# Kernel tuning notes

Measured on AMD Instinct MI355X. Metric: run time of the kernel, lower is better.

Reference implementation:

```python
import jax, jax.numpy as jnp
import numpy as np

SHAPES = ((8, 24, 24), (4, 12, 12), (2, 6, 6), (1, 3, 3))  # (D, H, W) per level
D_MODEL = 256
N_HEADS = 8
HEAD_DIM = D_MODEL // N_HEADS
N_LEVELS = 4
N_POINTS = 4
N_LAYERS = 6
D_FFN = 1024


def setup_inputs():
    key = jax.random.key(0)
    ks = iter(jax.random.split(key, 64))
    def rn(shape, s=1.0):
        return jax.random.normal(next(ks), shape, jnp.float32) * s
    inp = {}
    for i, (D, H, W) in enumerate(SHAPES):
        inp[f'src{i}'] = rn((2, 4, D_MODEL, D, H, W))
        inp[f'pos{i}'] = rn((2, 4, D_MODEL, D, H, W), 0.1)
    HLP3 = N_HEADS * N_LEVELS * N_POINTS * 3
    HLP = N_HEADS * N_LEVELS * N_POINTS
    L = N_LAYERS
    inp['level_embed'] = rn((N_LEVELS, D_MODEL), 0.02)
    inp['W_off'] = rn((L, D_MODEL, HLP3), 0.01)
    inp['b_off'] = rn((L, HLP3), 0.5)
    inp['W_attn'] = rn((L, D_MODEL, HLP), 0.02)
    inp['b_attn'] = jnp.zeros((L, HLP), jnp.float32)
    inp['W_val'] = rn((L, D_MODEL, D_MODEL), 0.02)
    inp['b_val'] = jnp.zeros((L, D_MODEL), jnp.float32)
    inp['W_out'] = rn((L, D_MODEL, D_MODEL), 0.02)
    inp['b_out'] = jnp.zeros((L, D_MODEL), jnp.float32)
    inp['g1'] = jnp.ones((L, D_MODEL), jnp.float32)
    inp['be1'] = jnp.zeros((L, D_MODEL), jnp.float32)
    inp['W1'] = rn((L, D_MODEL, D_FFN), 0.02)
    inp['b1'] = jnp.zeros((L, D_FFN), jnp.float32)
    inp['W2'] = rn((L, D_FFN, D_MODEL), 0.02)
    inp['b2'] = jnp.zeros((L, D_MODEL), jnp.float32)
    inp['g2'] = jnp.ones((L, D_MODEL), jnp.float32)
    inp['be2'] = jnp.zeros((L, D_MODEL), jnp.float32)
    return inp


def _layer_norm(x, g, b):
    m = jnp.mean(x, -1, keepdims=True)
    v = jnp.mean((x - m) ** 2, -1, keepdims=True)
    return (x - m) * jax.lax.rsqrt(v + 1e-5) * g + b


def _sample_level(v, loc, aw, D, H, W):
    # v: (B, nH, D*H*W, hd)   loc: (B, Lq, nH, P, 3) in [0,1] as (x,y,z)
    # aw: (B, Lq, nH, P) attention weights for this level
    # Trilinear sampling matching grid_sample(align_corners=False, padding_mode='zeros').
    B, Lq, nH, P, _ = loc.shape
    hd = v.shape[-1]
    x = loc[..., 0] * W - 0.5
    y = loc[..., 1] * H - 0.5
    z = loc[..., 2] * D - 0.5
    x0, y0, z0 = jnp.floor(x), jnp.floor(y), jnp.floor(z)
    fx, fy, fz = x - x0, y - y0, z - z0
    awt = aw.transpose(0, 2, 1, 3)  # (B, nH, Lq, P)
    out = jnp.zeros((B, nH, Lq, hd), v.dtype)
    for dz in (0, 1):
        for dy in (0, 1):
            for dx in (0, 1):
                xi, yi, zi = x0 + dx, y0 + dy, z0 + dz
                w = (fx if dx else 1.0 - fx) * (fy if dy else 1.0 - fy) * (fz if dz else 1.0 - fz)
                valid = (xi >= 0) & (xi < W) & (yi >= 0) & (yi < H) & (zi >= 0) & (zi < D)
                w = (w * valid).transpose(0, 2, 1, 3) * awt  # fold attn weight in
                idx = ((jnp.clip(zi, 0, D - 1) * H + jnp.clip(yi, 0, H - 1)) * W
                       + jnp.clip(xi, 0, W - 1)).astype(jnp.int32)
                idx = idx.transpose(0, 2, 1, 3).reshape(B, nH, Lq * P)
                g = jnp.take_along_axis(v, idx[..., None], 2).reshape(B, nH, Lq, P, hd)
                out = out + jnp.einsum('bhqpc,bhqp->bhqc', g, w)
    return out


def _msda(q, x, ref, Woff, boff, Wat, bat, Wv, bv, Wo, bo):
    B, Lq, _ = q.shape
    value = (x @ Wv + bv).reshape(B, Lq, N_HEADS, HEAD_DIM)
    off = (q @ Woff + boff).reshape(B, Lq, N_HEADS, N_LEVELS, N_POINTS, 3)
    attn = jax.nn.softmax((q @ Wat + bat).reshape(B, Lq, N_HEADS, N_LEVELS * N_POINTS), -1)
    attn = attn.reshape(B, Lq, N_HEADS, N_LEVELS, N_POINTS)
    # offset normalizer in (x, y, z) = (W, H, D) order per level
    norm = jnp.array([[W, H, D] for (D, H, W) in SHAPES], dtype=q.dtype)
    loc = ref[:, :, None, :, None, :] + off / norm[None, None, None, :, None, :]
    out = jnp.zeros((B, N_HEADS, Lq, HEAD_DIM), q.dtype)
    start = 0
    for lv, (D, H, W) in enumerate(SHAPES):
        n = D * H * W
        v_l = value[:, start:start + n].transpose(0, 2, 1, 3)  # (B, nH, n, hd)
        fn = jax.checkpoint(lambda v_, l_, a_, D=D, H=H, W=W: _sample_level(v_, l_, a_, D, H, W))
        out = out + fn(v_l, loc[:, :, :, lv], attn[:, :, :, lv])
        start += n
    return out.transpose(0, 2, 1, 3).reshape(B, Lq, D_MODEL) @ Wo + bo


def _forward(src0, src1, src2, src3, pos0, pos1, pos2, pos3, level_embed,
             W_off, b_off, W_attn, b_attn, W_val, b_val, W_out, b_out,
             g1, be1, W1, b1, W2, b2, g2, be2):
    srcs = [src0, src1, src2, src3]
    poss = [pos0, pos1, pos2, pos3]
    bs, nf = src0.shape[0], src0.shape[1]
    xs, ps = [], []
    for lvl in range(N_LEVELS):
        s, p = srcs[lvl], poss[lvl]
        b, n, c = s.shape[:3]
        xs.append(s.reshape(b, n, c, -1).transpose(0, 1, 3, 2))
        ps.append(p.reshape(b, n, c, -1).transpose(0, 1, 3, 2) + level_embed[lvl])
    x = jnp.concatenate(xs, 2)    # (bs, nf, Len, C)
    pos = jnp.concatenate(ps, 2)
    Len = x.shape[2]
    B = bs * nf
    x = x.reshape(B, Len, D_MODEL)
    pos = pos.reshape(B, Len, D_MODEL)
    # reference points; masks are all-False so valid_ratios == 1
    refs = []
    for (D, H, W) in SHAPES:
        rz, ry, rx = jnp.meshgrid(
            (jnp.arange(D, dtype=jnp.float32) + 0.5) / D,
            (jnp.arange(H, dtype=jnp.float32) + 0.5) / H,
            (jnp.arange(W, dtype=jnp.float32) + 0.5) / W,
            indexing='ij')
        refs.append(jnp.stack([rx.ravel(), ry.ravel(), rz.ravel()], -1))
    ref = jnp.concatenate(refs, 0)  # (Len, 3)
    ref = jnp.broadcast_to(ref[None, :, None, :], (B, Len, N_LEVELS, 3))
    for l in range(N_LAYERS):
        q = x + pos
        a = _msda(q, x, ref, W_off[l], b_off[l], W_attn[l], b_attn[l],
                  W_val[l], b_val[l], W_out[l], b_out[l])
        x = _layer_norm(x + a, g1[l], be1[l])
        ff = jax.nn.relu(x @ W1[l] + b1[l]) @ W2[l] + b2[l]
        x = _layer_norm(x + ff, g2[l], be2[l])
    return x.reshape(bs, nf, Len, D_MODEL)


def reference(src0, src1, src2, src3, pos0, pos1, pos2, pos3, level_embed,
              W_off, b_off, W_attn, b_attn, W_val, b_val, W_out, b_out,
              g1, be1, W1, b1, W2, b2, g2, be2):
    return _forward(src0, src1, src2, src3, pos0, pos1, pos2, pos3, level_embed,
                    W_off, b_off, W_attn, b_attn, W_val, b_val, W_out, b_out,
                    g1, be1, W1, b1, W2, b2, g2, be2)
```

## Files before the change

kernel.cpp:

```cpp
#include <hip/hip_runtime.h>

constexpr int LEN = 5265;
constexpr long NTOK = 8L * LEN;

typedef float f32x4 __attribute__((ext_vector_type(4)));
typedef unsigned int u32x4 __attribute__((ext_vector_type(4)));

static __device__ __forceinline__ unsigned short f2bf(float f) {
    unsigned u = __float_as_uint(f);
    unsigned r = (u + 0x7FFFu + ((u >> 16) & 1u)) >> 16;
    return (unsigned short)r;
}
static __device__ __forceinline__ float uasf(unsigned u) { return __uint_as_float(u); }

__global__ __launch_bounds__(256) void pack_kernel(
    const float* __restrict__ s0, const float* __restrict__ s1,
    const float* __restrict__ s2, const float* __restrict__ s3,
    const float* __restrict__ p0, const float* __restrict__ p1,
    const float* __restrict__ p2, const float* __restrict__ p3,
    const float* __restrict__ lev,
    float* __restrict__ x, float* __restrict__ pos,
    unsigned short* __restrict__ xbf, unsigned short* __restrict__ qbf)
{
    long t = (long)blockIdx.x * 256 + threadIdx.x;
    if (t >= NTOK * 256) return;
    int c = (int)(t & 255);
    long r = t >> 8;
    int q = (int)(r % LEN);
    int B = (int)(r / LEN);
    int lvl, base, n;
    const float *sp, *pp;
    if (q < 4608)      { lvl = 0; base = 0;    n = 4608; sp = s0; pp = p0; }
    else if (q < 5184) { lvl = 1; base = 4608; n = 576;  sp = s1; pp = p1; }
    else if (q < 5256) { lvl = 2; base = 5184; n = 72;   sp = s2; pp = p2; }
    else               { lvl = 3; base = 5256; n = 9;    sp = s3; pp = p3; }
    int s = q - base;
    long si = ((long)B * 256 + c) * n + s;
    float xv = sp[si];
    float pv = pp[si] + lev[lvl * 256 + c];
    x[t] = xv;
    pos[t] = pv;
    xbf[t] = f2bf(xv);
    qbf[t] = f2bf(xv + pv);
}

__global__ __launch_bounds__(64) void ref_kernel(float* __restrict__ refb)
{
    int q = blockIdx.x * 64 + threadIdx.x;
    if (q >= LEN) return;
    int base, D_, H_, W_;
    if (q < 4608)      { base = 0;    D_ = 8; H_ = 24; W_ = 24; }
    else if (q < 5184) { base = 4608; D_ = 4; H_ = 12; W_ = 12; }
    else if (q < 5256) { base = 5184; D_ = 2; H_ = 6;  W_ = 6;  }
    else               { base = 5256; D_ = 1; H_ = 3;  W_ = 3;  }
    int s = q - base;
    int hw = H_ * W_;
    int z = s / hw; int rem = s - z * hw;
    int y = rem / W_; int xx = rem - y * W_;
    refb[q * 3 + 0] = (xx + 0.5f) / (float)W_;
    refb[q * 3 + 1] = (y + 0.5f) / (float)H_;
    refb[q * 3 + 2] = (z + 0.5f) / (float)D_;
}

__global__ __launch_bounds__(256) void wtrans_kernel(
    const float* __restrict__ src, unsigned short* __restrict__ dst, int K, int N)
{
    __shared__ float t[32][33];
    const int k0 = blockIdx.x * 32, n0 = blockIdx.y * 32;
    const long off = (long)blockIdx.z * K * N;
    src += off; dst += off;
    const int tx = threadIdx.x, ty = threadIdx.y;
    for (int i = ty; i < 32; i += 8)
        t[i][tx] = src[(long)(k0 + i) * N + n0 + tx];
    __syncthreads();
    for (int i = ty; i < 32; i += 8)
        dst[(long)(n0 + i) * K + k0 + tx] = f2bf(t[tx][i]);
}

static __device__ __forceinline__ int swz(int m) { return (m ^ (m >> 2)) & 3; }

template<bool OUTBF, bool RELU>
__global__ __launch_bounds__(256) void mfma_gemm(
    const unsigned short* __restrict__ A, const unsigned short* __restrict__ Wt,
    const float* __restrict__ bias, void* __restrict__ Cv, int M, int K, int N)
{
    __shared__ u32x4 a_l[512];
    __shared__ u32x4 b_l[512];
    const int tid = threadIdx.x;
    const int row0 = blockIdx.x * 128;
    const int col0 = blockIdx.y * 128;
    const int wave = tid >> 6, lane = tid & 63;
    const int wr = wave >> 1, wc = wave & 1;
    const int l15 = lane & 15, l4 = lane >> 4;

    f32x4 acc[4][4];
#pragma unroll
    for (int i = 0; i < 4; ++i)
#pragma unroll
        for (int j = 0; j < 4; ++j) acc[i][j] = (f32x4){0.f, 0.f, 0.f, 0.f};

    const int sm0 = tid >> 2, sk = tid & 3;
    const int ar0 = row0 + sm0, ar1 = ar0 + 64;
    const int br0 = col0 + sm0, br1 = br0 + 64;
    const int sw0 = sk ^ swz(sm0);
    const int slot0 = sm0 * 4 + sw0;
    const int slot1 = (sm0 + 64) * 4 + sw0;

    for (int k0 = 0; k0 < K; k0 += 32) {
        u32x4 av0 = {0, 0, 0, 0}, av1 = {0, 0, 0, 0};
        if (ar0 < M) av0 = *(const u32x4*)&A[(long)ar0 * K + k0 + sk * 8];
        if (ar1 < M) av1 = *(const u32x4*)&A[(long)ar1 * K + k0 + sk * 8];
        const u32x4 bv0 = *(const u32x4*)&Wt[(long)br0 * K + k0 + sk * 8];
        const u32x4 bv1 = *(const u32x4*)&Wt[(long)br1 * K + k0 + sk * 8];
        __syncthreads();
        a_l[slot0] = av0;
        a_l[slot1] = av1;
        b_l[slot0] = bv0;
        b_l[slot1] = bv1;
        __syncthreads();
        u32x4 af[4], bfr[4];
#pragma unroll
        for (int i = 0; i < 4; ++i) {
            const int m = wr * 64 + i * 16 + l15;
            af[i] = a_l[m * 4 + (l4 ^ swz(m))];
            const int n = wc * 64 + i * 16 + l15;
            bfr[i] = b_l[n * 4 + (l4 ^ swz(n))];
        }
#pragma unroll
        for (int i = 0; i < 4; ++i)
#pragma unroll
            for (int j = 0; j < 4; ++j)
                asm volatile("v_mfma_f32_16x16x32_bf16 %0, %1, %2, %0"
                             : "+v"(acc[i][j]) : "v"(af[i]), "v"(bfr[j]));
    }

    float* Cf = (float*)Cv;
    unsigned short* Cb = (unsigned short*)Cv;
    const int cb = col0 + wc * 64;
    float bj[4];
#pragma unroll
    for (int j = 0; j < 4; ++j) bj[j] = bias[cb + j * 16 + l15];
#pragma unroll
    for (int i = 0; i < 4; ++i) {
        const int rb = row0 + wr * 64 + i * 16 + l4 * 4;
#pragma unroll
        for (int r = 0; r < 4; ++r) {
            const int row = rb + r;
            if (row < M) {
#pragma unroll
                for (int j = 0; j < 4; ++j) {
                    const int col = cb + j * 16 + l15;
                    float v = acc[i][j][r] + bj[j];
                    if (RELU) v = fmaxf(v, 0.f);
                    if (OUTBF) Cb[(long)row * N + col] = f2bf(v);
                    else       Cf[(long)row * N + col] = v;
                }
            }
        }
    }
}

__global__ __launch_bounds__(256) void msda_sample_kernel(
    const unsigned short* __restrict__ value,
    const float* __restrict__ offb,
    const float* __restrict__ attnl,
    const float* __restrict__ refb,
    unsigned short* __restrict__ outb)
{
    __shared__ float2 s_wi[32][130];
    const int tid = threadIdx.x;
    const long gid0 = (long)blockIdx.x * 32;

#pragma unroll
    for (int jj = 0; jj < 2; ++jj) {
        const int j = tid + jj * 256;
        const int g = j >> 4, pt = j & 15;
        const long gg = gid0 + g;
        const int h = (int)(gg & 7);
        const long bq = gg >> 3;
        const int q = (int)(bq % LEN);
        const int b = (int)(bq / LEN);

        const float* lg = &attnl[bq * 128 + h * 16];
        float mx = lg[0];
#pragma unroll
        for (int k = 1; k < 16; ++k) mx = fmaxf(mx, lg[k]);
        float den = 0.f;
#pragma unroll
        for (int k = 0; k < 16; ++k) den += __expf(lg[k] - mx);
        const float aw = __expf(lg[pt] - mx) / den;

        const int lvl = pt >> 2;
        int D_, H_, W_, base;
        if (lvl == 0)      { D_ = 8; H_ = 24; W_ = 24; base = 0; }
        else if (lvl == 1) { D_ = 4; H_ = 12; W_ = 12; base = 4608; }
        else if (lvl == 2) { D_ = 2; H_ = 6;  W_ = 6;  base = 5184; }
        else               { D_ = 1; H_ = 3;  W_ = 3;  base = 5256; }
        const float fW = (float)W_, fH = (float)H_, fD = (float)D_;

        const float* op = &offb[(bq * 8 + h) * 48 + pt * 3];
        const float X = (refb[q * 3 + 0] + op[0] / fW) * fW - 0.5f;
        const float Y = (refb[q * 3 + 1] + op[1] / fH) * fH - 0.5f;
        const float Z = (refb[q * 3 + 2] + op[2] / fD) * fD - 0.5f;
        const float x0f = floorf(X), y0f = floorf(Y), z0f = floorf(Z);
        const float fx = X - x0f, fy = Y - y0f, fz = Z - z0f;
        const int x0 = (int)x0f, y0 = (int)y0f, z0 = (int)z0f;
#pragma unroll
        for (int c = 0; c < 8; ++c) {
            const int dx = c & 1, dy = (c >> 1) & 1, dz = c >> 2;
            const int xi = x0 + dx, yi = y0 + dy, zi = z0 + dz;
            float w = (dx ? fx : 1.f - fx) * (dy ? fy : 1.f - fy) * (dz ? fz : 1.f - fz);
            const bool valid = (xi >= 0) && (xi < W_) && (yi >= 0) && (yi < H_) &&
                               (zi >= 0) && (zi < D_);
            const int xc = min(max(xi, 0), W_ - 1);
            const int yc = min(max(yi, 0), H_ - 1);
            const int zc = min(max(zi, 0), D_ - 1);
            const int n = (zc * H_ + yc) * W_ + xc;
            const int idx32 = (int)(((long)b * LEN + base + n) * 256) + h * 32;
            s_wi[g][pt * 8 + c] = make_float2(valid ? w * aw : 0.f,
                                              __int_as_float(idx32));
        }
    }
    __syncthreads();

    const int g = tid >> 3, d4 = tid & 7;
    const long gg = gid0 + g;
    float a0 = 0.f, a1 = 0.f, a2 = 0.f, a3 = 0.f;
#pragma unroll 4
    for (int i = 0; i < 128; ++i) {
        const float2 wi = s_wi[g][i];
        const float w = wi.x;
        const int idx = __float_as_int(wi.y);
        const uint2 v = *(const uint2*)&value[(long)idx + d4 * 4];
        a0 += w * uasf(v.x << 16);
        a1 += w * uasf(v.x & 0xffff0000u);
        a2 += w * uasf(v.y << 16);
        a3 += w * uasf(v.y & 0xffff0000u);
    }
    ushort4 o;
    o.x = f2bf(a0); o.y = f2bf(a1); o.z = f2bf(a2); o.w = f2bf(a3);
    *(ushort4*)&outb[gg * 32 + d4 * 4] = o;
}

__global__ __launch_bounds__(256) void resid_ln_kernel(
    float* __restrict__ x, const float* __restrict__ r, const float* __restrict__ pos,
    const float* __restrict__ g, const float* __restrict__ be,
    unsigned short* __restrict__ xbf, unsigned short* __restrict__ qbf)
{
    const long tok = (long)blockIdx.x * 4 + (threadIdx.x >> 6);
    const int lane = threadIdx.x & 63;
    if (tok >= NTOK) return;
    const float4 xv = *(const float4*)&x[tok * 256 + lane * 4];
    const float4 rv = *(const float4*)&r[tok * 256 + lane * 4];
    float s0 = xv.x + rv.x, s1 = xv.y + rv.y, s2 = xv.z + rv.z, s3 = xv.w + rv.w;
    float sum = s0 + s1 + s2 + s3;
#pragma unroll
    for (int o = 32; o > 0; o >>= 1) sum += __shfl_xor(sum, o);
    const float mean = sum * (1.f / 256.f);
    const float d0 = s0 - mean, d1 = s1 - mean, d2 = s2 - mean, d3 = s3 - mean;
    float vs = d0 * d0 + d1 * d1 + d2 * d2 + d3 * d3;
#pragma unroll
    for (int o = 32; o > 0; o >>= 1) vs += __shfl_xor(vs, o);
    const float rstd = rsqrtf(vs * (1.f / 256.f) + 1e-5f);
    float4 o4;
    o4.x = d0 * rstd * g[lane * 4 + 0] + be[lane * 4 + 0];
    o4.y = d1 * rstd * g[lane * 4 + 1] + be[lane * 4 + 1];
    o4.z = d2 * rstd * g[lane * 4 + 2] + be[lane * 4 + 2];
    o4.w = d3 * rstd * g[lane * 4 + 3] + be[lane * 4 + 3];
    *(float4*)&x[tok * 256 + lane * 4] = o4;
    ushort4 xb;
    xb.x = f2bf(o4.x); xb.y = f2bf(o4.y); xb.z = f2bf(o4.z); xb.w = f2bf(o4.w);
    *(ushort4*)&xbf[tok * 256 + lane * 4] = xb;
    const float4 pv = *(const float4*)&pos[tok * 256 + lane * 4];
    ushort4 qb;
    qb.x = f2bf(o4.x + pv.x); qb.y = f2bf(o4.y + pv.y);
    qb.z = f2bf(o4.z + pv.z); qb.w = f2bf(o4.w + pv.w);
    *(ushort4*)&qbf[tok * 256 + lane * 4] = qb;
}

extern "C" void kernel_launch(void* const* d_in, const int* in_sizes, int n_in,
                              void* d_out, int out_size, void* d_ws, size_t ws_size,
                              hipStream_t stream)
{
    (void)n_in; (void)out_size; (void)ws_size;
    const float* src[4];
    const float* posin[4];
    const bool interleaved = (in_sizes[1] == in_sizes[0]);
    for (int i = 0; i < 4; ++i) {
        if (interleaved) { src[i] = (const float*)d_in[2 * i]; posin[i] = (const float*)d_in[2 * i + 1]; }
        else             { src[i] = (const float*)d_in[i];     posin[i] = (const float*)d_in[4 + i]; }
    }
    const float* lev    = (const float*)d_in[8];
    const float* W_off  = (const float*)d_in[9];
    const float* b_off  = (const float*)d_in[10];
    const float* W_attn = (const float*)d_in[11];
    const float* b_attn = (const float*)d_in[12];
    const float* W_val  = (const float*)d_in[13];
    const float* b_val  = (const float*)d_in[14];
    const float* W_out  = (const float*)d_in[15];
    const float* b_out  = (const float*)d_in[16];
    const float* g1     = (const float*)d_in[17];
    const float* be1    = (const float*)d_in[18];
    const float* W1     = (const float*)d_in[19];
    const float* b1     = (const float*)d_in[20];
    const float* W2     = (const float*)d_in[21];
    const float* b2     = (const float*)d_in[22];
    const float* g2     = (const float*)d_in[23];
    const float* be2    = (const float*)d_in[24];

    float* xbuf = (float*)d_out;
    char* p = (char*)d_ws;
    float* posb = (float*)p;            p += NTOK * 256 * 4;
    float* tmp  = (float*)p;
    unsigned short* valueb = (unsigned short*)tmp;
                                        p += NTOK * 256 * 4;
    float* offb  = (float*)p;           p += NTOK * 384 * 4;
    float* attnb = (float*)p;
    unsigned short* msdabf = (unsigned short*)attnb;
                                        p += NTOK * 128 * 4;
    unsigned short* hidden = (unsigned short*)offb;
    unsigned short* xbf = (unsigned short*)p;  p += NTOK * 256 * 2;
    unsigned short* qbf = (unsigned short*)p;  p += NTOK * 256 * 2;
    unsigned short* wt_val  = (unsigned short*)p;  p += 6L * 256 * 256 * 2;
    unsigned short* wt_off  = (unsigned short*)p;  p += 6L * 384 * 256 * 2;
    unsigned short* wt_attn = (unsigned short*)p;  p += 6L * 128 * 256 * 2;
    unsigned short* wt_out  = (unsigned short*)p;  p += 6L * 256 * 256 * 2;
    unsigned short* wt_w1   = (unsigned short*)p;  p += 6L * 1024 * 256 * 2;
    unsigned short* wt_w2   = (unsigned short*)p;  p += 6L * 256 * 1024 * 2;
    float* refb = (float*)p;            p += LEN * 3 * 4;

    pack_kernel<<<(int)((NTOK * 256) / 256), 256, 0, stream>>>(
        src[0], src[1], src[2], src[3], posin[0], posin[1], posin[2], posin[3],
        lev, xbuf, posb, xbf, qbf);
    ref_kernel<<<(LEN + 63) / 64, 64, 0, stream>>>(refb);
    dim3 tb(32, 8);
    wtrans_kernel<<<dim3(8, 8, 6),  tb, 0, stream>>>(W_val,  wt_val,  256, 256);
    wtrans_kernel<<<dim3(8, 12, 6), tb, 0, stream>>>(W_off,  wt_off,  256, 384);
    wtrans_kernel<<<dim3(8, 4, 6),  tb, 0, stream>>>(W_attn, wt_attn, 256, 128);
    wtrans_kernel<<<dim3(8, 8, 6),  tb, 0, stream>>>(W_out,  wt_out,  256, 256);
    wtrans_kernel<<<dim3(8, 32, 6), tb, 0, stream>>>(W1,     wt_w1,   256, 1024);
    wtrans_kernel<<<dim3(32, 8, 6), tb, 0, stream>>>(W2,     wt_w2,   1024, 256);

    const int MT = (int)((NTOK + 127) / 128);
    for (int l = 0; l < 6; ++l) {
        mfma_gemm<true, false><<<dim3(MT, 2), 256, 0, stream>>>(
            xbf, wt_val + (long)l * 65536, b_val + l * 256, valueb, (int)NTOK, 256, 256);
        mfma_gemm<false, false><<<dim3(MT, 3), 256, 0, stream>>>(
            qbf, wt_off + (long)l * 98304, b_off + l * 384, offb, (int)NTOK, 256, 384);
        mfma_gemm<false, false><<<dim3(MT, 1), 256, 0, stream>>>(
            qbf, wt_attn + (long)l * 32768, b_attn + l * 128, attnb, (int)NTOK, 256, 128);
        msda_sample_kernel<<<(int)(NTOK / 4), 256, 0, stream>>>(
            valueb, offb, attnb, refb, msdabf);
        mfma_gemm<false, false><<<dim3(MT, 2), 256, 0, stream>>>(
            msdabf, wt_out + (long)l * 65536, b_out + l * 256, tmp, (int)NTOK, 256, 256);
        resid_ln_kernel<<<(int)((NTOK + 3) / 4), 256, 0, stream>>>(
            xbuf, tmp, posb, g1 + l * 256, be1 + l * 256, xbf, qbf);
        mfma_gemm<true, true><<<dim3(MT, 8), 256, 0, stream>>>(
            xbf, wt_w1 + (long)l * 262144, b1 + l * 1024, hidden, (int)NTOK, 256, 1024);
        mfma_gemm<false, false><<<dim3(MT, 2), 256, 0, stream>>>(
            hidden, wt_w2 + (long)l * 262144, b2 + l * 256, tmp, (int)NTOK, 1024, 256);
        resid_ln_kernel<<<(int)((NTOK + 3) / 4), 256, 0, stream>>>(
            xbuf, tmp, posb, g2 + l * 256, be2 + l * 256, xbf, qbf);
    }
}
```

Baseline: 2.821 ms.

## Fuse offset/attn GEMMs, use direct-to-LDS loads, pack sampling indices, skip unused q

Concatenates the offset and attention-weight projection weights so a single GEMM with N=512 writes both into one buffer, using a split bias. The GEMM tile loads switch to global_load_lds, which writes global data straight into LDS without passing through registers. Sampling weights and token indices are packed into 32-bit words (fp16 weight plus 16-bit token index), and the gather loop is fully unrolled. The first layernorm no longer writes the q buffer it does not need. These changes cut launches, register traffic and LDS footprint, at the cost of fp16 weight precision and a 16-bit token index limit (42120 tokens fits).

```diff
diff --git a/kernel.cpp b/kernel.cpp
--- a/kernel.cpp
+++ b/kernel.cpp
@@ -1,4 +1,5 @@
 #include <hip/hip_runtime.h>
+#include <hip/hip_fp16.h>
 
 constexpr int LEN = 5265;
 constexpr long NTOK = 8L * LEN;
@@ -12,6 +13,17 @@
     return (unsigned short)r;
 }
 static __device__ __forceinline__ float uasf(unsigned u) { return __uint_as_float(u); }
+
+#if __has_builtin(__builtin_amdgcn_global_load_lds)
+#define HAS_GLL 1
+static __device__ __forceinline__ void gll16(const void* g, void* l) {
+    __builtin_amdgcn_global_load_lds(
+        (const __attribute__((address_space(1))) void*)g,
+        (__attribute__((address_space(3))) void*)l, 16, 0, 0);
+}
+#else
+#define HAS_GLL 0
+#endif
 
 __global__ __launch_bounds__(256) void pack_kernel(
     const float* __restrict__ s0, const float* __restrict__ s1,
@@ -63,12 +75,13 @@
 }
 
 __global__ __launch_bounds__(256) void wtrans_kernel(
-    const float* __restrict__ src, unsigned short* __restrict__ dst, int K, int N)
+    const float* __restrict__ src, unsigned short* __restrict__ dst,
+    int K, int N, long dstLS)
 {
     __shared__ float t[32][33];
     const int k0 = blockIdx.x * 32, n0 = blockIdx.y * 32;
-    const long off = (long)blockIdx.z * K * N;
-    src += off; dst += off;
+    src += (long)blockIdx.z * K * N;
+    dst += (long)blockIdx.z * dstLS;
     const int tx = threadIdx.x, ty = threadIdx.y;
     for (int i = ty; i < 32; i += 8)
         t[i][tx] = src[(long)(k0 + i) * N + n0 + tx];
@@ -82,7 +95,8 @@
 template<bool OUTBF, bool RELU>
 __global__ __launch_bounds__(256) void mfma_gemm(
     const unsigned short* __restrict__ A, const unsigned short* __restrict__ Wt,
-    const float* __restrict__ bias, void* __restrict__ Cv, int M, int K, int N)
+    const float* __restrict__ bias, const float* __restrict__ bias2, int nb0,
+    void* __restrict__ Cv, int M, int K, int N)
 {
     __shared__ u32x4 a_l[512];
     __shared__ u32x4 b_l[512];
@@ -100,23 +114,27 @@
         for (int j = 0; j < 4; ++j) acc[i][j] = (f32x4){0.f, 0.f, 0.f, 0.f};
 
     const int sm0 = tid >> 2, sk = tid & 3;
-    const int ar0 = row0 + sm0, ar1 = ar0 + 64;
-    const int br0 = col0 + sm0, br1 = br0 + 64;
-    const int sw0 = sk ^ swz(sm0);
-    const int slot0 = sm0 * 4 + sw0;
-    const int slot1 = (sm0 + 64) * 4 + sw0;
+    const int swk = (sk ^ swz(sm0)) * 8;
+    const int arA0 = min(row0 + sm0, M - 1);
+    const int arA1 = min(row0 + sm0 + 64, M - 1);
+    const unsigned short* gA0 = A  + (long)arA0 * K + swk;
+    const unsigned short* gA1 = A  + (long)arA1 * K + swk;
+    const unsigned short* gB0 = Wt + (long)(col0 + sm0) * K + swk;
+    const unsigned short* gB1 = Wt + (long)(col0 + sm0 + 64) * K + swk;
 
     for (int k0 = 0; k0 < K; k0 += 32) {
-        u32x4 av0 = {0, 0, 0, 0}, av1 = {0, 0, 0, 0};
-        if (ar0 < M) av0 = *(const u32x4*)&A[(long)ar0 * K + k0 + sk * 8];
-        if (ar1 < M) av1 = *(const u32x4*)&A[(long)ar1 * K + k0 + sk * 8];
-        const u32x4 bv0 = *(const u32x4*)&Wt[(long)br0 * K + k0 + sk * 8];
-        const u32x4 bv1 = *(const u32x4*)&Wt[(long)br1 * K + k0 + sk * 8];
         __syncthreads();
-        a_l[slot0] = av0;
-        a_l[slot1] = av1;
-        b_l[slot0] = bv0;
-        b_l[slot1] = bv1;
+#if HAS_GLL
+        gll16(gA0 + k0, &a_l[wave * 64]);
+        gll16(gA1 + k0, &a_l[256 + wave * 64]);
+        gll16(gB0 + k0, &b_l[wave * 64]);
+        gll16(gB1 + k0, &b_l[256 + wave * 64]);
+#else
+        a_l[tid]       = *(const u32x4*)(gA0 + k0);
+        a_l[256 + tid] = *(const u32x4*)(gA1 + k0);
+        b_l[tid]       = *(const u32x4*)(gB0 + k0);
+        b_l[256 + tid] = *(const u32x4*)(gB1 + k0);
+#endif
         __syncthreads();
         u32x4 af[4], bfr[4];
 #pragma unroll
@@ -139,7 +157,10 @@
     const int cb = col0 + wc * 64;
     float bj[4];
 #pragma unroll
-    for (int j = 0; j < 4; ++j) bj[j] = bias[cb + j * 16 + l15];
+    for (int j = 0; j < 4; ++j) {
+        const int col = cb + j * 16 + l15;
+        bj[j] = (col < nb0) ? bias[col] : bias2[col - nb0];
+    }
 #pragma unroll
     for (int i = 0; i < 4; ++i) {
         const int rb = row0 + wr * 64 + i * 16 + l4 * 4;
@@ -162,12 +183,11 @@
 
 __global__ __launch_bounds__(256) void msda_sample_kernel(
     const unsigned short* __restrict__ value,
-    const float* __restrict__ offb,
-    const float* __restrict__ attnl,
+    const float* __restrict__ obuf,
     const float* __restrict__ refb,
     unsigned short* __restrict__ outb)
 {
-    __shared__ float2 s_wi[32][130];
+    __shared__ unsigned s_wi[32][8][17];
     const int tid = threadIdx.x;
     const long gid0 = (long)blockIdx.x * 32;
 
@@ -177,11 +197,11 @@
         const int g = j >> 4, pt = j & 15;
         const long gg = gid0 + g;
         const int h = (int)(gg & 7);
-        const long bq = gg >> 3;
-        const int q = (int)(bq % LEN);
-        const int b = (int)(bq / LEN);
-
-        const float* lg = &attnl[bq * 128 + h * 16];
+        const long tok = gg >> 3;
+        const int q = (int)(tok % LEN);
+        const int b = (int)(tok / LEN);
+
+        const float* lg = &obuf[tok * 512 + 384 + h * 16];
         float mx = lg[0];
 #pragma unroll
         for (int k = 1; k < 16; ++k) mx = fmaxf(mx, lg[k]);
@@ -198,7 +218,7 @@
         else               { D_ = 1; H_ = 3;  W_ = 3;  base = 5256; }
         const float fW = (float)W_, fH = (float)H_, fD = (float)D_;
 
-        const float* op = &offb[(bq * 8 + h) * 48 + pt * 3];
+        const float* op = &obuf[tok * 512 + h * 48 + pt * 3];
         const float X = (refb[q * 3 + 0] + op[0] / fW) * fW - 0.5f;
         const float Y = (refb[q * 3 + 1] + op[1] / fH) * fH - 0.5f;
         const float Z = (refb[q * 3 + 2] + op[2] / fD) * fD - 0.5f;
@@ -216,32 +236,39 @@
             const int yc = min(max(yi, 0), H_ - 1);
             const int zc = min(max(zi, 0), D_ - 1);
             const int n = (zc * H_ + yc) * W_ + xc;
-            const int idx32 = (int)(((long)b * LEN + base + n) * 256) + h * 32;
-            s_wi[g][pt * 8 + c] = make_float2(valid ? w * aw : 0.f,
-                                              __int_as_float(idx32));
+            const unsigned short ti = (unsigned short)(b * LEN + base + n);
+            const unsigned short hw =
+                __half_as_ushort(__float2half_rn(valid ? w * aw : 0.f));
+            s_wi[g][c][pt] = ((unsigned)ti << 16) | (unsigned)hw;
         }
     }
     __syncthreads();
 
     const int g = tid >> 3, d4 = tid & 7;
     const long gg = gid0 + g;
+    const int h = (int)(gg & 7);
+    const char* vbase = (const char*)value + h * 64 + d4 * 8;
+    const unsigned* sp = &s_wi[g][0][0];
     float a0 = 0.f, a1 = 0.f, a2 = 0.f, a3 = 0.f;
-#pragma unroll 4
-    for (int i = 0; i < 128; ++i) {
-        const float2 wi = s_wi[g][i];
-        const float w = wi.x;
-        const int idx = __float_as_int(wi.y);
-        const uint2 v = *(const uint2*)&value[(long)idx + d4 * 4];
-        a0 += w * uasf(v.x << 16);
-        a1 += w * uasf(v.x & 0xffff0000u);
-        a2 += w * uasf(v.y << 16);
-        a3 += w * uasf(v.y & 0xffff0000u);
+#pragma unroll
+    for (int c = 0; c < 8; ++c) {
+#pragma unroll
+        for (int pt = 0; pt < 16; ++pt) {
+            const unsigned word = sp[c * 17 + pt];
+            const float w = __half2float(__ushort_as_half((unsigned short)word));
+            const uint2 v = *(const uint2*)(vbase + ((word >> 16) << 9));
+            a0 += w * uasf(v.x << 16);
+            a1 += w * uasf(v.x & 0xffff0000u);
+            a2 += w * uasf(v.y << 16);
+            a3 += w * uasf(v.y & 0xffff0000u);
+        }
     }
     ushort4 o;
     o.x = f2bf(a0); o.y = f2bf(a1); o.z = f2bf(a2); o.w = f2bf(a3);
     *(ushort4*)&outb[gg * 32 + d4 * 4] = o;
 }
 
+template<bool NEEDQ>
 __global__ __launch_bounds__(256) void resid_ln_kernel(
     float* __restrict__ x, const float* __restrict__ r, const float* __restrict__ pos,
     const float* __restrict__ g, const float* __restrict__ be,
@@ -271,11 +298,13 @@
     ushort4 xb;
     xb.x = f2bf(o4.x); xb.y = f2bf(o4.y); xb.z = f2bf(o4.z); xb.w = f2bf(o4.w);
     *(ushort4*)&xbf[tok * 256 + lane * 4] = xb;
-    const float4 pv = *(const float4*)&pos[tok * 256 + lane * 4];
-    ushort4 qb;
-    qb.x = f2bf(o4.x + pv.x); qb.y = f2bf(o4.y + pv.y);
-    qb.z = f2bf(o4.z + pv.z); qb.w = f2bf(o4.w + pv.w);
-    *(ushort4*)&qbf[tok * 256 + lane * 4] = qb;
+    if (NEEDQ) {
+        const float4 pv = *(const float4*)&pos[tok * 256 + lane * 4];
+        ushort4 qb;
+        qb.x = f2bf(o4.x + pv.x); qb.y = f2bf(o4.y + pv.y);
+        qb.z = f2bf(o4.z + pv.z); qb.w = f2bf(o4.w + pv.w);
+        *(ushort4*)&qbf[tok * 256 + lane * 4] = qb;
+    }
 }
 
 extern "C" void kernel_launch(void* const* d_in, const int* in_sizes, int n_in,
@@ -314,19 +343,17 @@
     float* tmp  = (float*)p;
     unsigned short* valueb = (unsigned short*)tmp;
                                         p += NTOK * 256 * 4;
-    float* offb  = (float*)p;           p += NTOK * 384 * 4;
-    float* attnb = (float*)p;
-    unsigned short* msdabf = (unsigned short*)attnb;
-                                        p += NTOK * 128 * 4;
-    unsigned short* hidden = (unsigned short*)offb;
-    unsigned short* xbf = (unsigned short*)p;  p += NTOK * 256 * 2;
-    unsigned short* qbf = (unsigned short*)p;  p += NTOK * 256 * 2;
-    unsigned short* wt_val  = (unsigned short*)p;  p += 6L * 256 * 256 * 2;
-    unsigned short* wt_off  = (unsigned short*)p;  p += 6L * 384 * 256 * 2;
-    unsigned short* wt_attn = (unsigned short*)p;  p += 6L * 128 * 256 * 2;
-    unsigned short* wt_out  = (unsigned short*)p;  p += 6L * 256 * 256 * 2;
-    unsigned short* wt_w1   = (unsigned short*)p;  p += 6L * 1024 * 256 * 2;
-    unsigned short* wt_w2   = (unsigned short*)p;  p += 6L * 256 * 1024 * 2;
+    float* obuf = (float*)p;
+    unsigned short* hidden = (unsigned short*)obuf;
+                                        p += NTOK * 512 * 4;
+    unsigned short* msdabf = (unsigned short*)p;  p += NTOK * 256 * 2;
+    unsigned short* xbf    = (unsigned short*)p;  p += NTOK * 256 * 2;
+    unsigned short* qbf    = (unsigned short*)p;  p += NTOK * 256 * 2;
+    unsigned short* wt_val = (unsigned short*)p;  p += 6L * 256 * 256 * 2;
+    unsigned short* wt_oa  = (unsigned short*)p;  p += 6L * 512 * 256 * 2;
+    unsigned short* wt_out = (unsigned short*)p;  p += 6L * 256 * 256 * 2;
+    unsigned short* wt_w1  = (unsigned short*)p;  p += 6L * 1024 * 256 * 2;
+    unsigned short* wt_w2  = (unsigned short*)p;  p += 6L * 256 * 1024 * 2;
     float* refb = (float*)p;            p += LEN * 3 * 4;
 
     pack_kernel<<<(int)((NTOK * 256) / 256), 256, 0, stream>>>(
@@ -334,32 +361,36 @@
         lev, xbuf, posb, xbf, qbf);
     ref_kernel<<<(LEN + 63) / 64, 64, 0, stream>>>(refb);
     dim3 tb(32, 8);
-    wtrans_kernel<<<dim3(8, 8, 6),  tb, 0, stream>>>(W_val,  wt_val,  256, 256);
-    wtrans_kernel<<<dim3(8, 12, 6), tb, 0, stream>>>(W_off,  wt_off,  256, 384);
-    wtrans_kernel<<<dim3(8, 4, 6),  tb, 0, stream>>>(W_attn, wt_attn, 256, 128);
-    wtrans_kernel<<<dim3(8, 8, 6),  tb, 0, stream>>>(W_out,  wt_out,  256, 256);
-    wtrans_kernel<<<dim3(8, 32, 6), tb, 0, stream>>>(W1,     wt_w1,   256, 1024);
-    wtrans_kernel<<<dim3(32, 8, 6), tb, 0, stream>>>(W2,     wt_w2,   1024, 256);
+    wtrans_kernel<<<dim3(8, 8, 6),  tb, 0, stream>>>(W_val,  wt_val, 256, 256,  65536);
+    wtrans_kernel<<<dim3(8, 12, 6), tb, 0, stream>>>(W_off,  wt_oa,  256, 384,  131072);
+    wtrans_kernel<<<dim3(8, 4, 6),  tb, 0, stream>>>(W_attn, wt_oa + 384 * 256, 256, 128, 131072);
+    wtrans_kernel<<<dim3(8, 8, 6),  tb, 0, stream>>>(W_out,  wt_out, 256, 256,  65536);
+    wtrans_kernel<<<dim3(8, 32, 6), tb, 0, stream>>>(W1,     wt_w1,  256, 1024, 262144);
+    wtrans_kernel<<<dim3(32, 8, 6), tb, 0, stream>>>(W2,     wt_w2,  1024, 256, 262144);
 
     const int MT = (int)((NTOK + 127) / 128);
+    const int BIG = 1 << 30;
     for (int l = 0; l < 6; ++l) {
         mfma_gemm<true, false><<<dim3(MT, 2), 256, 0, stream>>>(
-            xbf, wt_val + (long)l * 65536, b_val + l * 256, valueb, (int)NTOK, 256, 256);
-        mfma_gemm<false, false><<<dim3(MT, 3), 256, 0, stream>>>(
-            qbf, wt_off + (long)l * 98304, b_off + l * 384, offb, (int)NTOK, 256, 384);
-        mfma_gemm<false, false><<<dim3(MT, 1), 256, 0, stream>>>(
-            qbf, wt_attn + (long)l * 32768, b_attn + l * 128, attnb, (int)NTOK, 256, 128);
+            xbf, wt_val + (long)l * 65536, b_val + l * 256, b_val + l * 256, BIG,
+            valueb, (int)NTOK, 256, 256);
+        mfma_gemm<false, false><<<dim3(MT, 4), 256, 0, stream>>>(
+            qbf, wt_oa + (long)l * 131072, b_off + l * 384, b_attn + l * 128, 384,
+            obuf, (int)NTOK, 256, 512);
         msda_sample_kernel<<<(int)(NTOK / 4), 256, 0, stream>>>(
-            valueb, offb, attnb, refb, msdabf);
+            valueb, obuf, refb, msdabf);
         mfma_gemm<false, false><<<dim3(MT, 2), 256, 0, stream>>>(
-            msdabf, wt_out + (long)l * 65536, b_out + l * 256, tmp, (int)NTOK, 256, 256);
-        resid_ln_kernel<<<(int)((NTOK + 3) / 4), 256, 0, stream>>>(
+            msdabf, wt_out + (long)l * 65536, b_out + l * 256, b_out + l * 256, BIG,
+            tmp, (int)NTOK, 256, 256);
+        resid_ln_kernel<false><<<(int)((NTOK + 3) / 4), 256, 0, stream>>>(
             xbuf, tmp, posb, g1 + l * 256, be1 + l * 256, xbf, qbf);
         mfma_gemm<true, true><<<dim3(MT, 8), 256, 0, stream>>>(
-            xbf, wt_w1 + (long)l * 262144, b1 + l * 1024, hidden, (int)NTOK, 256, 1024);
+            xbf, wt_w1 + (long)l * 262144, b1 + l * 1024, b1 + l * 1024, BIG,
+            hidden, (int)NTOK, 256, 1024);
         mfma_gemm<false, false><<<dim3(MT, 2), 256, 0, stream>>>(
-            hidden, wt_w2 + (long)l * 262144, b2 + l * 256, tmp, (int)NTOK, 1024, 256);
-        resid_ln_kernel<<<(int)((NTOK + 3) / 4), 256, 0, stream>>>(
+            hidden, wt_w2 + (long)l * 262144, b2 + l * 256, b2 + l * 256, BIG,
+            tmp, (int)NTOK, 1024, 256);
+        resid_ln_kernel<true><<<(int)((NTOK + 3) / 4), 256, 0, stream>>>(
             xbuf, tmp, posb, g2 + l * 256, be2 + l * 256, xbf, qbf);
     }
 }
```

Result: faster. 2.593 ms (-8.1%).
